# Kernel tuning notes

Hardware: AMD Instinct MI355X
Metric: run time of the kernel (lower is better)

## Reference

```python
import jax, jax.numpy as jnp
import numpy as np

HEADS = 16


def setup_inputs() -> dict:
    key = jax.random.key(0)
    k1, k2, k3, k4, k5, k6 = jax.random.split(key, 6)
    L, B, H = 1024, 8, 2048
    dk = H // HEADS
    std = 1.0 / np.sqrt(H)
    return {
        "query": jax.random.normal(k1, (B, H), dtype=jnp.float32),
        "feed_hiddens": jax.random.normal(k2, (L, B, H), dtype=jnp.float32),
        "values": jax.random.normal(k3, (L, B, H), dtype=jnp.float32),
        # additive-attention params (reconstructed from forward's shape constraints)
        "attn_w": jax.random.normal(k4, (2 * dk, H), dtype=jnp.float32) * std,
        "bias": jax.random.normal(k5, (H,), dtype=jnp.float32) * std,
        "score": jax.random.normal(k6, (H, 1), dtype=jnp.float32) * std,
    }


def reference(query, feed_hiddens, values, attn_w, bias, score):
    L, B, H = feed_hiddens.shape
    dk = H // HEADS
    # q: [B, h, 1, dk]; k, v: [B, h, L, dk]
    q = query.reshape(B, HEADS, 1, dk)
    k = feed_hiddens.reshape(L, B, HEADS, dk).transpose(1, 2, 0, 3)
    v = values.reshape(L, B, HEADS, dk).transpose(1, 2, 0, 3)
    # cat([q_rep, k], -1) @ attn_w  ==  q @ Wq + k @ Wk  (avoids the repeat/concat blowup)
    Wq, Wk = attn_w[:dk], attn_w[dk:]
    energy = jax.nn.relu(q @ Wq + k @ Wk + bias)        # [B, h, L, H]
    logits = (energy @ score).transpose(0, 1, 3, 2)     # [B, h, 1, L]
    a = jax.nn.softmax(logits, axis=-1)
    out = (a @ v).reshape(B, H)[None]                   # [1, B, H]
    return out
```

## Files before the change

kernel.cpp:

```cpp
#include <hip/hip_runtime.h>
#include <hip/hip_bf16.h>
#include <hip/hip_fp8.h>

#define HEADS 16
#define B_    8
#define H_    2048
#define L_    1024
#define DK    128

typedef __attribute__((ext_vector_type(8))) int   i32x8;
typedef __attribute__((ext_vector_type(4))) int   i32x4;
typedef __attribute__((ext_vector_type(4))) float f32x4;

__device__ __forceinline__ unsigned u8e4m3(float x) {
  __hip_fp8_e4m3 f8(x);
  return (unsigned)f8.__x;
}

__device__ __forceinline__ void gload_lds16(const void* g, void* l) {
  __builtin_amdgcn_global_load_lds(
      (const __attribute__((address_space(1))) void*)g,
      (__attribute__((address_space(3))) void*)l, 16, 0, 0);
}

__global__ void __launch_bounds__(256)
prep_kernel(const float* __restrict__ query,
            const float* __restrict__ attn_w,
            const float* __restrict__ bias,
            const float* __restrict__ score,
            float2* __restrict__ qs2,
            unsigned char* __restrict__ wk8) {
  const int tid = threadIdx.x;
  if (blockIdx.x < 128) {
    const int jt = blockIdx.x & 7;
    const int bg = blockIdx.x >> 3;
    __shared__ float qv[8][DK];
    for (int i = tid; i < 8 * DK; i += 256) {
      const int bh = bg * 8 + (i >> 7);
      const int d  = i & 127;
      const int b = bh >> 4, head = bh & 15;
      qv[i >> 7][d] = query[b * H_ + head * DK + d];
    }
    __syncthreads();
    const int j = jt * 256 + tid;
    const float bj = bias[j];
    const float sj = score[j] * (1.0f / 64.0f);
    float acc[8];
#pragma unroll
    for (int u = 0; u < 8; ++u) acc[u] = bj;
    for (int d = 0; d < DK; ++d) {
      const float wv = attn_w[d * H_ + j];
#pragma unroll
      for (int u = 0; u < 8; ++u) acc[u] += qv[u][d] * wv;
    }
#pragma unroll
    for (int u = 0; u < 8; ++u) {
      float2 t; t.x = 64.0f * acc[u]; t.y = sj;
      qs2[(size_t)(bg * 8 + u) * H_ + j] = t;
    }
  } else {
    const int t0 = (blockIdx.x - 128) * 256 + tid;
    for (int tt = t0; tt < 8192; tt += 4096) {
      const int l  = tt & 63;
      const int nc = tt >> 6;
      const int n  = nc * 16 + (l & 15);
      const int k0 = (l >> 4) * 32;
#pragma unroll
      for (int half = 0; half < 2; ++half) {
        unsigned w[4];
#pragma unroll
        for (int j = 0; j < 4; ++j) {
          unsigned v = 0;
#pragma unroll
          for (int byt = 0; byt < 4; ++byt) {
            const int i = half * 16 + j * 4 + byt;
            const float x = 64.0f * attn_w[(size_t)(DK + k0 + i) * H_ + n];
            v |= u8e4m3(x) << (8 * byt);
          }
          w[j] = v;
        }
        uint4 q; q.x = w[0]; q.y = w[1]; q.z = w[2]; q.w = w[3];
        *(uint4*)(wk8 + (size_t)nc * 2048 + half * 1024 + l * 16) = q;
      }
    }
  }
}

__global__ void __launch_bounds__(256, 2)
logits_kernel(const float* __restrict__ feed,
              const unsigned char* __restrict__ wk8,
              const float2* __restrict__ qs2,
              float* __restrict__ logits) {
  const int ltile = blockIdx.x;
  const int bh    = blockIdx.y;
  const int b     = bh >> 4;
  const int head  = bh & 15;
  const int tid   = threadIdx.x;
  const int wave  = tid >> 6;
  const int lane  = tid & 63;
  const int row   = lane & 15;
  const int g     = lane >> 4;

  __shared__ unsigned char ring[4][16384];
  __shared__ float2 qs[H_];

#pragma unroll
  for (int u = 0; u < 8; ++u)
    qs[tid + 256 * u] = qs2[(size_t)bh * H_ + tid + 256 * u];

  i32x8 aF[4];
#pragma unroll
  for (int s = 0; s < 4; ++s) {
    const int l = ltile * 256 + wave * 64 + s * 16 + row;
    const float* fh = feed + (size_t)l * (B_ * H_) + b * H_ + head * DK + g * 32;
    i32x8 af;
#pragma unroll
    for (int j = 0; j < 8; ++j) {
      float4 x = *(const float4*)(fh + j * 4);
      unsigned v = u8e4m3(x.x) | (u8e4m3(x.y) << 8) |
                   (u8e4m3(x.z) << 16) | (u8e4m3(x.w) << 24);
      af[j] = (int)v;
    }
    aF[s] = af;
  }
  __syncthreads();

  const char* wkb   = (const char*)wk8;
  char*       ringb = (char*)ring;
  const int   seg0  = wave * 4096;

#pragma unroll
  for (int ph = 0; ph < 2; ++ph) {
#pragma unroll
    for (int i = 0; i < 4; ++i)
      gload_lds16(wkb + (size_t)ph * 16384 + seg0 + i * 1024 + lane * 16,
                  ringb + ph * 16384 + seg0 + i * 1024);
  }

  float lacc[4][4] = {};

#pragma unroll 1
  for (int p = 0; p < 16; ++p) {
    const int pf = (p + 2 < 16) ? p + 2 : 15;
    const int ws = ((p + 2) & 3) * 16384;
#pragma unroll
    for (int i = 0; i < 4; ++i)
      gload_lds16(wkb + (size_t)pf * 16384 + seg0 + i * 1024 + lane * 16,
                  ringb + ws + seg0 + i * 1024);

    __builtin_amdgcn_sched_barrier(0);
    asm volatile("s_waitcnt vmcnt(8)" ::: "memory");
    __builtin_amdgcn_s_barrier();
    __builtin_amdgcn_sched_barrier(0);

    const char* rs = ringb + (p & 3) * 16384;
#pragma unroll
    for (int cc = 0; cc < 8; ++cc) {
      const char* rc = rs + cc * 2048 + lane * 16;
      i32x4 lo = *(const i32x4*)(rc);
      i32x4 hi = *(const i32x4*)(rc + 1024);
      i32x8 b8;
      b8[0] = lo[0]; b8[1] = lo[1]; b8[2] = lo[2]; b8[3] = lo[3];
      b8[4] = hi[0]; b8[5] = hi[1]; b8[6] = hi[2]; b8[7] = hi[3];
      const float2 q2 = qs[(8 * p + cc) * 16 + row];
      const float qx = q2.x, qy = q2.y;

      f32x4 d0 = {qx, qx, qx, qx};
      f32x4 d1 = {qx, qx, qx, qx};
      f32x4 d2 = {qx, qx, qx, qx};
      f32x4 d3 = {qx, qx, qx, qx};
      d0 = __builtin_amdgcn_mfma_scale_f32_16x16x128_f8f6f4(
             aF[0], b8, d0, 0, 0, 0, 0x7F7F7F7F, 0, 0x7F7F7F7F);
      d1 = __builtin_amdgcn_mfma_scale_f32_16x16x128_f8f6f4(
             aF[1], b8, d1, 0, 0, 0, 0x7F7F7F7F, 0, 0x7F7F7F7F);
      d2 = __builtin_amdgcn_mfma_scale_f32_16x16x128_f8f6f4(
             aF[2], b8, d2, 0, 0, 0, 0x7F7F7F7F, 0, 0x7F7F7F7F);
      d3 = __builtin_amdgcn_mfma_scale_f32_16x16x128_f8f6f4(
             aF[3], b8, d3, 0, 0, 0, 0x7F7F7F7F, 0, 0x7F7F7F7F);

#pragma unroll
      for (int i = 0; i < 4; ++i) {
        lacc[0][i] += fmaxf(d0[i], 0.f) * qy;
        lacc[1][i] += fmaxf(d1[i], 0.f) * qy;
        lacc[2][i] += fmaxf(d2[i], 0.f) * qy;
        lacc[3][i] += fmaxf(d3[i], 0.f) * qy;
      }
    }
  }

#pragma unroll
  for (int s = 0; s < 4; ++s) {
#pragma unroll
    for (int i = 0; i < 4; ++i) {
      float v = lacc[s][i];
#pragma unroll
      for (int off = 1; off < 16; off <<= 1) v += __shfl_xor(v, off);
      lacc[s][i] = v;
    }
  }
  if (row == 0) {
#pragma unroll
    for (int s = 0; s < 4; ++s) {
      const int base = bh * L_ + ltile * 256 + wave * 64 + s * 16 + g * 4;
#pragma unroll
      for (int i = 0; i < 4; ++i) logits[base + i] = lacc[s][i];
    }
  }
}

__global__ void __launch_bounds__(256)
softmax_pv_kernel(const float* __restrict__ logits,
                  const float* __restrict__ values,
                  float* __restrict__ out) {
  const int bh    = blockIdx.x;
  const int dpart = blockIdx.y;
  const int b     = bh >> 4;
  const int head  = bh & 15;
  const int tid   = threadIdx.x;

  __shared__ float  sl[L_];
  __shared__ float  sred[4];
  __shared__ float  sscal;
  __shared__ float4 pacc[32][8];

  float m = -1e30f;
  for (int i = tid; i < L_; i += 256) {
    float v = logits[(size_t)bh * L_ + i];
    sl[i] = v;
    m = fmaxf(m, v);
  }
#pragma unroll
  for (int off = 32; off > 0; off >>= 1) m = fmaxf(m, __shfl_xor(m, off));
  if ((tid & 63) == 0) sred[tid >> 6] = m;
  __syncthreads();
  if (tid == 0) {
    float mm = fmaxf(fmaxf(sred[0], sred[1]), fmaxf(sred[2], sred[3]));
    sscal = mm;
  }
  __syncthreads();
  const float mx = sscal;

  float s = 0.f;
  for (int i = tid; i < L_; i += 256) {
    float e = __expf(sl[i] - mx);
    sl[i] = e;
    s += e;
  }
#pragma unroll
  for (int off = 32; off > 0; off >>= 1) s += __shfl_xor(s, off);
  if ((tid & 63) == 0) sred[tid >> 6] = s;
  __syncthreads();
  if (tid == 0) {
    sscal = 1.0f / ((sred[0] + sred[1]) + (sred[2] + sred[3]));
  }
  __syncthreads();
  const float inv = sscal;

  const int dq4  = tid & 7;
  const int lsub = tid >> 3;
  const float4* vp = (const float4*)(values + (size_t)b * H_ + head * DK + dpart * 32) + dq4;
  float4 acc = {0.f, 0.f, 0.f, 0.f};
  for (int ll = lsub; ll < L_; ll += 32) {
    const float w = sl[ll];
    float4 v = vp[(size_t)ll * (B_ * H_ / 4)];
    acc.x += w * v.x; acc.y += w * v.y; acc.z += w * v.z; acc.w += w * v.w;
  }
  pacc[lsub][dq4] = acc;
  __syncthreads();
  if (tid < 64) {
    const int q = tid & 7, k = tid >> 3;
    float4 a0 = pacc[k][q], a1 = pacc[k + 8][q], a2 = pacc[k + 16][q], a3 = pacc[k + 24][q];
    float4 r;
    r.x = (a0.x + a1.x) + (a2.x + a3.x);
    r.y = (a0.y + a1.y) + (a2.y + a3.y);
    r.z = (a0.z + a1.z) + (a2.z + a3.z);
    r.w = (a0.w + a1.w) + (a2.w + a3.w);
    pacc[k][q] = r;
  }
  __syncthreads();
  if (tid < 8) {
    float4 t = {0.f, 0.f, 0.f, 0.f};
#pragma unroll
    for (int k = 0; k < 8; ++k) {
      float4 a = pacc[k][tid];
      t.x += a.x; t.y += a.y; t.z += a.z; t.w += a.w;
    }
    t.x *= inv; t.y *= inv; t.z *= inv; t.w *= inv;
    *(float4*)(out + (size_t)b * H_ + head * DK + dpart * 32 + tid * 4) = t;
  }
}

extern "C" void kernel_launch(void* const* d_in, const int* in_sizes, int n_in,
                              void* d_out, int out_size, void* d_ws, size_t ws_size,
                              hipStream_t stream) {
  const float* query  = (const float*)d_in[0];
  const float* feed   = (const float*)d_in[1];
  const float* values = (const float*)d_in[2];
  const float* attn_w = (const float*)d_in[3];
  const float* bias   = (const float*)d_in[4];
  const float* score  = (const float*)d_in[5];
  float* out = (float*)d_out;

  float2*        qs2    = (float2*)d_ws;
  unsigned char* wk8    = (unsigned char*)d_ws + (size_t)(B_ * HEADS * H_) * sizeof(float2);
  float*         logits = (float*)(wk8 + (size_t)H_ * DK);

  prep_kernel<<<144, 256, 0, stream>>>(query, attn_w, bias, score, qs2, wk8);
  logits_kernel<<<dim3(L_ / 256, B_ * HEADS), 256, 0, stream>>>(feed, wk8, qs2, logits);
  softmax_pv_kernel<<<dim3(B_ * HEADS, 4), 256, 0, stream>>>(logits, values, out);
}
```

Before: 80.66 us.

## Split logits kernel over N halves with larger L tiles per block

The logits kernel now gives each block 512 L rows (8 MFMA row tiles per wave) and only half of the H output columns. A new grid z dimension covers the two column halves, and their partial logits are summed in the softmax kernel. Each staged weight tile is now reused across twice as many rows, cutting weight traffic per row. The cost is higher register pressure (8 fragments plus 32 accumulators), loss of the 2-blocks-per-CU launch bound, and an extra logits buffer read.

After: 124.7 us. 1.55x slower.

```diff
diff --git a/kernel.cpp b/kernel.cpp
--- a/kernel.cpp
+++ b/kernel.cpp
@@ -86,13 +86,14 @@
   }
 }
 
-__global__ void __launch_bounds__(256, 2)
+__global__ void __launch_bounds__(256)
 logits_kernel(const float* __restrict__ feed,
               const unsigned char* __restrict__ wk8,
               const float2* __restrict__ qs2,
               float* __restrict__ logits) {
   const int ltile = blockIdx.x;
   const int bh    = blockIdx.y;
+  const int nblk  = blockIdx.z;
   const int b     = bh >> 4;
   const int head  = bh & 15;
   const int tid   = threadIdx.x;
@@ -102,16 +103,16 @@
   const int g     = lane >> 4;
 
   __shared__ unsigned char ring[4][16384];
-  __shared__ float2 qs[H_];
-
-#pragma unroll
-  for (int u = 0; u < 8; ++u)
-    qs[tid + 256 * u] = qs2[(size_t)bh * H_ + tid + 256 * u];
-
-  i32x8 aF[4];
-#pragma unroll
-  for (int s = 0; s < 4; ++s) {
-    const int l = ltile * 256 + wave * 64 + s * 16 + row;
+  __shared__ float2 qs[1024];
+
+#pragma unroll
+  for (int u = 0; u < 4; ++u)
+    qs[tid + 256 * u] = qs2[(size_t)bh * H_ + nblk * 1024 + tid + 256 * u];
+
+  i32x8 aF[8];
+#pragma unroll
+  for (int s = 0; s < 8; ++s) {
+    const int l = ltile * 512 + wave * 128 + s * 16 + row;
     const float* fh = feed + (size_t)l * (B_ * H_) + b * H_ + head * DK + g * 32;
     i32x8 af;
 #pragma unroll
@@ -125,7 +126,7 @@
   }
   __syncthreads();
 
-  const char* wkb   = (const char*)wk8;
+  const char* wkb   = (const char*)wk8 + (size_t)nblk * 131072;
   char*       ringb = (char*)ring;
   const int   seg0  = wave * 4096;
 
@@ -137,11 +138,11 @@
                   ringb + ph * 16384 + seg0 + i * 1024);
   }
 
-  float lacc[4][4] = {};
+  float lacc[8][4] = {};
 
 #pragma unroll 1
-  for (int p = 0; p < 16; ++p) {
-    const int pf = (p + 2 < 16) ? p + 2 : 15;
+  for (int p = 0; p < 8; ++p) {
+    const int pf = (p + 2 < 8) ? p + 2 : 7;
     const int ws = ((p + 2) & 3) * 16384;
 #pragma unroll
     for (int i = 0; i < 4; ++i)
@@ -165,31 +166,24 @@
       const float2 q2 = qs[(8 * p + cc) * 16 + row];
       const float qx = q2.x, qy = q2.y;
 
-      f32x4 d0 = {qx, qx, qx, qx};
-      f32x4 d1 = {qx, qx, qx, qx};
-      f32x4 d2 = {qx, qx, qx, qx};
-      f32x4 d3 = {qx, qx, qx, qx};
-      d0 = __builtin_amdgcn_mfma_scale_f32_16x16x128_f8f6f4(
-             aF[0], b8, d0, 0, 0, 0, 0x7F7F7F7F, 0, 0x7F7F7F7F);
-      d1 = __builtin_amdgcn_mfma_scale_f32_16x16x128_f8f6f4(
-             aF[1], b8, d1, 0, 0, 0, 0x7F7F7F7F, 0, 0x7F7F7F7F);
-      d2 = __builtin_amdgcn_mfma_scale_f32_16x16x128_f8f6f4(
-             aF[2], b8, d2, 0, 0, 0, 0x7F7F7F7F, 0, 0x7F7F7F7F);
-      d3 = __builtin_amdgcn_mfma_scale_f32_16x16x128_f8f6f4(
-             aF[3], b8, d3, 0, 0, 0, 0x7F7F7F7F, 0, 0x7F7F7F7F);
-
-#pragma unroll
-      for (int i = 0; i < 4; ++i) {
-        lacc[0][i] += fmaxf(d0[i], 0.f) * qy;
-        lacc[1][i] += fmaxf(d1[i], 0.f) * qy;
-        lacc[2][i] += fmaxf(d2[i], 0.f) * qy;
-        lacc[3][i] += fmaxf(d3[i], 0.f) * qy;
+      const f32x4 dini = {qx, qx, qx, qx};
+      f32x4 d[8];
+#pragma unroll
+      for (int s = 0; s < 8; ++s)
+        d[s] = __builtin_amdgcn_mfma_scale_f32_16x16x128_f8f6f4(
+                 aF[s], b8, dini, 0, 0, 0, 0x7F7F7F7F, 0, 0x7F7F7F7F);
+
+#pragma unroll
+      for (int s = 0; s < 8; ++s) {
+#pragma unroll
+        for (int i = 0; i < 4; ++i)
+          lacc[s][i] += fmaxf(d[s][i], 0.f) * qy;
       }
     }
   }
 
 #pragma unroll
-  for (int s = 0; s < 4; ++s) {
+  for (int s = 0; s < 8; ++s) {
 #pragma unroll
     for (int i = 0; i < 4; ++i) {
       float v = lacc[s][i];
@@ -199,11 +193,12 @@
     }
   }
   if (row == 0) {
-#pragma unroll
-    for (int s = 0; s < 4; ++s) {
-      const int base = bh * L_ + ltile * 256 + wave * 64 + s * 16 + g * 4;
-#pragma unroll
-      for (int i = 0; i < 4; ++i) logits[base + i] = lacc[s][i];
+    float* lout = logits + (size_t)nblk * (128 * L_);
+#pragma unroll
+    for (int s = 0; s < 8; ++s) {
+      const int base = bh * L_ + ltile * 512 + wave * 128 + s * 16 + g * 4;
+#pragma unroll
+      for (int i = 0; i < 4; ++i) lout[base + i] = lacc[s][i];
     }
   }
 }
@@ -225,7 +220,8 @@
 
   float m = -1e30f;
   for (int i = tid; i < L_; i += 256) {
-    float v = logits[(size_t)bh * L_ + i];
+    float v = logits[(size_t)bh * L_ + i] +
+              logits[(size_t)(128 * L_) + bh * L_ + i];
     sl[i] = v;
     m = fmaxf(m, v);
   }
@@ -306,6 +302,6 @@
   float*         logits = (float*)(wk8 + (size_t)H_ * DK);
 
   prep_kernel<<<144, 256, 0, stream>>>(query, attn_w, bias, score, qs2, wk8);
-  logits_kernel<<<dim3(L_ / 256, B_ * HEADS), 256, 0, stream>>>(feed, wk8, qs2, logits);
+  logits_kernel<<<dim3(L_ / 512, B_ * HEADS, 2), 256, 0, stream>>>(feed, wk8, qs2, logits);
   softmax_pv_kernel<<<dim3(B_ * HEADS, 4), 256, 0, stream>>>(logits, values, out);
 }
```
